# Performance work log

Measured on AMD Instinct MI355X. Metric: run time of the kernel, lower is better.

## Reference

```python
import jax, jax.numpy as jnp
import numpy as np

B, S, A, D, C = 64, 512, 8, 128, 1024
NUM_CLS = 34


def setup_inputs() -> dict:
    key = jax.random.key(0)
    k1, k2, k3, k4, k5 = jax.random.split(key, 5)
    word_repr = jax.random.normal(k1, (B, S, A, D), dtype=jnp.float32)
    anchor_cls = jax.random.randint(k2, (B, S, A), 0, NUM_CLS, dtype=jnp.int32)
    anchor_loc = jax.random.randint(k3, (B, S, A, 2), 0, 16, dtype=jnp.int32)
    # exactly C candidates per sentence so the view to [B, C, D] is valid
    batch_idx = jnp.repeat(jnp.arange(B, dtype=jnp.int32), C)
    wid = jax.random.randint(k4, (B * C,), 0, S, dtype=jnp.int32)
    aid = jax.random.randint(k5, (B * C,), 0, A, dtype=jnp.int32)
    candidates_idx = jnp.stack([batch_idx, wid, aid], axis=1)  # [B*C, 3]
    return {
        "word_repr": word_repr,
        "anchor_cls": anchor_cls,
        "anchor_loc": anchor_loc,
        "candidates_idx": candidates_idx,
        "batch_candidate_num": C,
    }


def reference(word_repr, anchor_cls, anchor_loc, candidates_idx, batch_candidate_num):
    Bb, Ss, Aa, Dd = word_repr.shape
    Cc = batch_candidate_num
    b, w, a = candidates_idx[:, 0], candidates_idx[:, 1], candidates_idx[:, 2]
    # multi-dim gather: [B*C, D]
    batch_candidates_repr = word_repr[b, w, a, :].reshape(Bb, Cc, Dd)
    batch_candidates_label = anchor_cls[b, w, a].reshape(Bb, Cc)
    candidate_loc = anchor_loc[b, w, a]  # [B*C, 2]
    # invalid candidate: start == end -> mask 0
    candidate_mask = (candidate_loc[:, 0] != candidate_loc[:, 1]).astype(
        word_repr.dtype
    ).reshape(Bb, Cc)
    candidate_len = jnp.sum(candidate_mask, axis=1)
    # nonzero=True: force len >= 1
    candidate_len = jnp.maximum(candidate_len, jnp.asarray(1, candidate_len.dtype))
    candidate_loc = candidate_loc.reshape(Bb, Cc, 2)
    batch_candidates_repr = batch_candidates_repr * candidate_mask[..., None]
    return (
        batch_candidates_repr,
        batch_candidates_label,
        batch_candidate_num,
        candidate_len,
        candidate_mask,
        candidate_loc,
    )
```

## Files before the change

### kernel.cpp

```cpp
#include <hip/hip_runtime.h>

#define BB   64
#define SS   512
#define AA   8
#define DD   128
#define CC   1024
#define NCAND (BB * CC)

#define OFF_REPR  0ULL
#define SZ_REPR   ((size_t)BB * CC * DD)
#define OFF_LABEL (OFF_REPR + SZ_REPR)
#define OFF_NUM   (OFF_LABEL + (size_t)BB * CC)
#define OFF_LEN   (OFF_NUM + 1ULL)
#define OFF_MASK  (OFF_LEN + (size_t)BB)
#define OFF_LOC   (OFF_MASK + (size_t)BB * CC)

__global__ __launch_bounds__(256) void fused_kernel(
    const float* __restrict__ word_repr,
    const int*   __restrict__ anchor_cls,
    const int*   __restrict__ anchor_loc,
    const int*   __restrict__ cand_idx,
    const int*   __restrict__ cnum,
    float*       __restrict__ out)
{
    const int tid  = threadIdx.x;
    const int lane = tid & 31;
    const int i    = blockIdx.x * 8 + (tid >> 5);

    const int b = cand_idx[3 * i + 0];
    const int w = cand_idx[3 * i + 1];
    const int a = cand_idx[3 * i + 2];
    const int base = (b * SS + w) * AA + a;

    const int2 loc = ((const int2*)anchor_loc)[base];
    const float m = (loc.x != loc.y) ? 1.0f : 0.0f;

    const float4 v = ((const float4*)word_repr)[(size_t)base * 32 + lane];
    float4 r;
    r.x = v.x * m; r.y = v.y * m; r.z = v.z * m; r.w = v.w * m;
    ((float4*)(out + OFF_REPR))[(size_t)i * 32 + lane] = r;

    if (lane == 0) {
        out[OFF_LABEL + i] = (float)anchor_cls[base];
        out[OFF_MASK  + i] = m;
        out[OFF_LOC + 2 * (size_t)i + 0] = (float)loc.x;
        out[OFF_LOC + 2 * (size_t)i + 1] = (float)loc.y;
    }

    if (blockIdx.x < BB) {
        const int bb = blockIdx.x;
        float msum = 0.0f;
#pragma unroll
        for (int j = 0; j < CC / 256; ++j) {
            const int c  = tid + j * 256;
            const int i2 = bb * CC + c;
            const int b2 = cand_idx[3 * i2 + 0];
            const int w2 = cand_idx[3 * i2 + 1];
            const int a2 = cand_idx[3 * i2 + 2];
            const int2 l2 = ((const int2*)anchor_loc)[(b2 * SS + w2) * AA + a2];
            msum += (l2.x != l2.y) ? 1.0f : 0.0f;
        }
#pragma unroll
        for (int off = 32; off > 0; off >>= 1)
            msum += __shfl_down(msum, off, 64);

        __shared__ float sm[4];
        if ((tid & 63) == 0) sm[tid >> 6] = msum;
        __syncthreads();
        if (tid == 0) {
            const float s = sm[0] + sm[1] + sm[2] + sm[3];
            out[OFF_LEN + bb] = fmaxf(s, 1.0f);
            if (bb == 0) out[OFF_NUM] = (float)(*cnum);
        }
    }
}

extern "C" void kernel_launch(void* const* d_in, const int* in_sizes, int n_in,
                              void* d_out, int out_size, void* d_ws, size_t ws_size,
                              hipStream_t stream) {
    const float* word_repr  = (const float*)d_in[0];
    const int*   anchor_cls = (const int*)  d_in[1];
    const int*   anchor_loc = (const int*)  d_in[2];
    const int*   cand_idx   = (const int*)  d_in[3];
    const int*   cnum       = (const int*)  d_in[4];
    float*       out        = (float*)      d_out;

    fused_kernel<<<dim3(NCAND / 8), dim3(256), 0, stream>>>(
        word_repr, anchor_cls, anchor_loc, cand_idx, cnum, out);
}
```

Before: 192.6 us.

## Process 16 candidates per block with nontemporal stores and coalesced side outputs

Each block now handles 16 candidates instead of 8. Each 16-thread group moves one 512-byte row using two vector loads per thread, and the output rows are written with nontemporal stores. The label, mask and location side outputs are staged in shared memory and written as contiguous coalesced runs instead of scattered single-lane stores. This cuts the block count and avoids caching streaming output, at the cost of an added __syncthreads in every block.

```diff
diff --git a/kernel.cpp b/kernel.cpp
--- a/kernel.cpp
+++ b/kernel.cpp
@@ -15,6 +15,8 @@
 #define OFF_MASK  (OFF_LEN + (size_t)BB)
 #define OFF_LOC   (OFF_MASK + (size_t)BB * CC)
 
+typedef float f32x4 __attribute__((ext_vector_type(4)));
+
 __global__ __launch_bounds__(256) void fused_kernel(
     const float* __restrict__ word_repr,
     const int*   __restrict__ anchor_cls,
@@ -23,9 +25,13 @@
     const int*   __restrict__ cnum,
     float*       __restrict__ out)
 {
-    const int tid  = threadIdx.x;
-    const int lane = tid & 31;
-    const int i    = blockIdx.x * 8 + (tid >> 5);
+    const int tid    = threadIdx.x;
+    const int lane16 = tid & 15;
+    const int g      = tid >> 4;
+    const int i0     = blockIdx.x * 16;
+    const int i      = i0 + g;
+
+    __shared__ float side[64];
 
     const int b = cand_idx[3 * i + 0];
     const int w = cand_idx[3 * i + 1];
@@ -35,16 +41,29 @@
     const int2 loc = ((const int2*)anchor_loc)[base];
     const float m = (loc.x != loc.y) ? 1.0f : 0.0f;
 
-    const float4 v = ((const float4*)word_repr)[(size_t)base * 32 + lane];
-    float4 r;
-    r.x = v.x * m; r.y = v.y * m; r.z = v.z * m; r.w = v.w * m;
-    ((float4*)(out + OFF_REPR))[(size_t)i * 32 + lane] = r;
+    const f32x4* src = (const f32x4*)word_repr + (size_t)base * 32;
+    const f32x4 v0 = src[lane16];
+    const f32x4 v1 = src[lane16 + 16];
 
-    if (lane == 0) {
-        out[OFF_LABEL + i] = (float)anchor_cls[base];
-        out[OFF_MASK  + i] = m;
-        out[OFF_LOC + 2 * (size_t)i + 0] = (float)loc.x;
-        out[OFF_LOC + 2 * (size_t)i + 1] = (float)loc.y;
+    f32x4* dst = (f32x4*)(out + OFF_REPR) + (size_t)i * 32;
+    __builtin_nontemporal_store(v0 * m, dst + lane16);
+    __builtin_nontemporal_store(v1 * m, dst + lane16 + 16);
+
+    if (lane16 == 0) {
+        side[g]           = (float)anchor_cls[base];
+        side[16 + g]      = m;
+        side[32 + 2 * g]  = (float)loc.x;
+        side[33 + 2 * g]  = (float)loc.y;
+    }
+    __syncthreads();
+
+    if (tid < 16) {
+        __builtin_nontemporal_store(side[tid], out + OFF_LABEL + i0 + tid);
+    } else if (tid < 32) {
+        __builtin_nontemporal_store(side[tid], out + OFF_MASK + i0 + (tid - 16));
+    } else if (tid < 64) {
+        __builtin_nontemporal_store(side[tid],
+                                    out + OFF_LOC + 2 * (size_t)i0 + (tid - 32));
     }
 
     if (blockIdx.x < BB) {
@@ -85,6 +104,6 @@
     const int*   cnum       = (const int*)  d_in[4];
     float*       out        = (float*)      d_out;
 
-    fused_kernel<<<dim3(NCAND / 8), dim3(256), 0, stream>>>(
+    fused_kernel<<<dim3(NCAND / 16), dim3(256), 0, stream>>>(
         word_repr, anchor_cls, anchor_loc, cand_idx, cnum, out);
 }
```

New measurement: 190.9 us. No clear change (-0.9%).
